# Performance work log

Measured on AMD Instinct MI355X. Metric: run time of the kernel, lower is better.

## Reference

```python
import jax, jax.numpy as jnp
import numpy as np
from jax import lax

T, B, C, H, W, NH = 4, 4, 512, 32, 32, 8
HD = C // NH  # head dim 64
EPS = 1e-5
TAU = 2.0

@jax.custom_vjp
def spike(x):
    # Heaviside forward (spikingjelly: x >= 0 -> 1)
    return (x >= 0.0).astype(x.dtype)

def _spike_fwd(x):
    return spike(x), x

def _spike_bwd(x, g):
    # sigmoid surrogate gradient, alpha=4.0 (spikingjelly default)
    s = jax.nn.sigmoid(4.0 * x)
    return (g * 4.0 * s * (1.0 - s),)

spike.defvjp(_spike_fwd, _spike_bwd)

def lif(x, v_th=1.0):
    # MultiStepLIFNode: tau=2, v_reset=0 (hard reset), detach_reset=True.
    # x: [T, ...]; sequential over T via scan.
    def step(v, xt):
        v = v + (xt - v) / TAU
        s = spike(v - v_th)
        v = v * (1.0 - lax.stop_gradient(s))  # detach_reset hard reset
        return v, s
    return lax.scan(step, jnp.zeros_like(x[0]), x)[1]

def bn(x, g, b, m, v):
    # eval-mode BatchNorm1d over channel axis 2 of [T,B,C,N]
    scale = g / jnp.sqrt(v + EPS)
    return (x - m[:, None]) * scale[:, None] + b[:, None]

def setup_inputs() -> dict:
    key = jax.random.key(0)
    ks = jax.random.split(key, 24)
    def w(k):
        return jax.random.normal(k, (C, C), jnp.float32) * (1.0 / np.sqrt(C))
    def bnp(k):
        k1, k2, k3, k4 = jax.random.split(k, 4)
        return (jax.random.normal(k1, (C,), jnp.float32) * 0.1 + 1.0,
                jax.random.normal(k2, (C,), jnp.float32) * 0.1,
                jax.random.normal(k3, (C,), jnp.float32) * 0.1,
                jax.random.uniform(k4, (C,), jnp.float32, 0.5, 1.5))
    q_g, q_b, q_m, q_v = bnp(ks[1])
    k_g, k_b, k_m, k_v = bnp(ks[3])
    v_g, v_b, v_m, v_v = bnp(ks[5])
    p_g, p_b, p_m, p_v = bnp(ks[7])
    return {
        'x': jax.random.normal(ks[0], (T, B, C, H, W), jnp.float32),
        'Wq': w(ks[10]), 'q_g': q_g, 'q_b': q_b, 'q_m': q_m, 'q_v': q_v,
        'Wk': w(ks[11]), 'k_g': k_g, 'k_b': k_b, 'k_m': k_m, 'k_v': k_v,
        'Wv': w(ks[12]), 'v_g': v_g, 'v_b': v_b, 'v_m': v_m, 'v_v': v_v,
        'Wp': w(ks[13]), 'bp': jax.random.normal(ks[14], (C,), jnp.float32) * 0.02,
        'p_g': p_g, 'p_b': p_b, 'p_m': p_m, 'p_v': p_v,
    }

def reference(x, Wq, q_g, q_b, q_m, q_v, Wk, k_g, k_b, k_m, k_v,
              Wv, v_g, v_b, v_m, v_v, Wp, bp, p_g, p_b, p_m, p_v):
    t, b, c, h, w = x.shape
    n = h * w
    xs = lif(x).reshape(t, b, c, n)  # proj_lif -> spikes in {0,1}

    def qkv_branch(Wt, g, bb, m, v):
        y = jnp.einsum('tbcn,dc->tbdn', xs, Wt)  # conv1x1
        y = lif(bn(y, g, bb, m, v))               # bn + lif
        # [T,B,C,N] -> [T,B,heads,N,head_dim]
        return y.reshape(t, b, NH, HD, n).transpose(0, 1, 2, 4, 3)

    q = qkv_branch(Wq, q_g, q_b, q_m, q_v)
    k = qkv_branch(Wk, k_g, k_b, k_m, k_v)
    v = qkv_branch(Wv, v_g, v_b, v_m, v_v)

    attn = jnp.einsum('tbhnd,tbhmd->tbhnm', q, k)           # q @ k^T (binary spikes)
    o = jnp.einsum('tbhnm,tbhmd->tbhnd', attn, v) * 0.125   # attn @ v * 0.125
    o = o.transpose(0, 1, 2, 4, 3).reshape(t, b, c, n)      # [T,B,C,N]
    o = lif(o, v_th=0.5)                                     # attn_lif

    y = jnp.einsum('tbcn,dc->tbdn', o, Wp) + bp[:, None]     # proj conv (bias)
    y = bn(y, p_g, p_b, p_m, p_v)
    return y.reshape(t, b, c, h, w)
```

## Files before the change

kernel.cpp:

```cpp
#include <hip/hip_runtime.h>
#include <hip/hip_bf16.h>
#include <stdint.h>

#define T_  4
#define B_  4
#define C_  512
#define N_  1024
#define NH_ 8
#define HD_ 64
#define NP_ 16384
#define EPS_ 1e-5f

typedef __bf16 bf16_t;
typedef __bf16 bf16x8 __attribute__((ext_vector_type(8)));
typedef float  f32x4  __attribute__((ext_vector_type(4)));
typedef unsigned short u16x4 __attribute__((ext_vector_type(4)));
typedef unsigned char  u8x4  __attribute__((ext_vector_type(4)));
typedef unsigned long long u64;
typedef unsigned int u32;

#define XS_OFF   0ULL
#define AHI_OFF  16777216ULL
#define ALO_OFF  18350080ULL
#define PHI_OFF  19922944ULL
#define PLO_OFF  20447232ULL
#define SC_OFF   20971520ULL
#define SH_OFF   20977664ULL
#define PSC_OFF  20983808ULL
#define PSH_OFF  20985856ULL
#define QS_OFF   20987904ULL
#define KB_OFF   37765120ULL
#define VB_OFF   38813696ULL
#define M2H_OFF  39862272ULL
#define M2L_OFF  40910848ULL

__global__ __launch_bounds__(256) void prep_kernel(
    const float* __restrict__ Wq, const float* __restrict__ Wk,
    const float* __restrict__ Wv, const float* __restrict__ Wp,
    const float* __restrict__ qg, const float* __restrict__ qb, const float* __restrict__ qm, const float* __restrict__ qv,
    const float* __restrict__ kg, const float* __restrict__ kb, const float* __restrict__ km, const float* __restrict__ kv,
    const float* __restrict__ vg, const float* __restrict__ vb, const float* __restrict__ vm, const float* __restrict__ vv,
    const float* __restrict__ bp,
    const float* __restrict__ pg, const float* __restrict__ pb, const float* __restrict__ pm, const float* __restrict__ pv,
    bf16_t* __restrict__ Ahi, bf16_t* __restrict__ Alo,
    bf16_t* __restrict__ Phi, bf16_t* __restrict__ Plo,
    float* __restrict__ scale, float* __restrict__ shift,
    float* __restrict__ pscale, float* __restrict__ pshift)
{
    const int i0 = blockIdx.x * 256 + threadIdx.x;
    const int stride = gridDim.x * 256;
    for (int idx = i0; idx < 1536 * 512; idx += stride) {
        int r = idx >> 9;
        int br = r >> 9;
        const float* W = (br == 0) ? Wq : (br == 1) ? Wk : Wv;
        float w = W[((r & 511) << 9) + (idx & 511)];
        bf16_t h = (bf16_t)w;
        Ahi[idx] = h;
        Alo[idx] = (bf16_t)(w - (float)h);
    }
    for (int idx = i0; idx < 512 * 512; idx += stride) {
        float w = Wp[idx];
        bf16_t h = (bf16_t)w;
        Phi[idx] = h;
        Plo[idx] = (bf16_t)(w - (float)h);
    }
    for (int idx = i0; idx < 1536; idx += stride) {
        int br = idx >> 9, d = idx & 511;
        const float* g  = (br == 0) ? qg : (br == 1) ? kg : vg;
        const float* bb = (br == 0) ? qb : (br == 1) ? kb : vb;
        const float* mm = (br == 0) ? qm : (br == 1) ? km : vm;
        const float* vr = (br == 0) ? qv : (br == 1) ? kv : vv;
        float sc = g[d] / sqrtf(vr[d] + EPS_);
        scale[idx] = sc;
        shift[idx] = bb[d] - mm[d] * sc;
    }
    for (int idx = i0; idx < 512; idx += stride) {
        float sc = pg[idx] / sqrtf(pv[idx] + EPS_);
        pscale[idx] = sc;
        pshift[idx] = (bp[idx] - pm[idx]) * sc + pb[idx];
    }
}

__global__ __launch_bounds__(256) void lif_x_kernel(const float* __restrict__ x,
                                                    bf16_t* __restrict__ xsT)
{
    __shared__ bf16_t St[64 * 72];
    const int tid = threadIdx.x;
    const int nl  = tid & 63;
    const int c4  = tid >> 6;
    const int n0 = blockIdx.x * 64;
    const int c0 = blockIdx.y * 64;
    const int b  = blockIdx.z;
    float v[16];
#pragma unroll
    for (int k = 0; k < 16; ++k) v[k] = 0.f;

    for (int t = 0; t < T_; ++t) {
        bf16x8 s0, s1;
#pragma unroll
        for (int k = 0; k < 16; ++k) {
            float xv = x[(size_t)((t * B_ + b) * C_ + (c0 + c4 * 16 + k)) * N_ + n0 + nl];
            float vn = v[k] + (xv - v[k]) * 0.5f;
            bool s = (vn >= 1.0f);
            v[k] = s ? 0.0f : vn;
            bf16_t sp = s ? (bf16_t)1.0f : (bf16_t)0.0f;
            if (k < 8) s0[k] = sp; else s1[k - 8] = sp;
        }
        __syncthreads();
        *(bf16x8*)&St[nl * 72 + c4 * 16]     = s0;
        *(bf16x8*)&St[nl * 72 + c4 * 16 + 8] = s1;
        __syncthreads();
#pragma unroll
        for (int it = 0; it < 2; ++it) {
            int id = it * 256 + tid;
            int row = id >> 3, sg = id & 7;
            *(bf16x8*)&xsT[((size_t)((t * B_ + b) << 10) + n0 + row) * C_ + c0 + sg * 8] =
                *(const bf16x8*)&St[row * 72 + sg * 8];
        }
    }
}

__global__ __launch_bounds__(256) void gemm_qkv_lif(
    const bf16_t* __restrict__ Ahi, const bf16_t* __restrict__ Alo,
    const bf16_t* __restrict__ xsT,
    const float* __restrict__ scale, const float* __restrict__ shift,
    bf16_t* __restrict__ qsT, u32* __restrict__ kbits, u32* __restrict__ vbits)
{
    __shared__ __align__(16) unsigned char smem[49152];

    const int tid  = threadIdx.x;
    const int lane = tid & 63;
    const int wv   = tid >> 6;
    const int wr   = wv >> 1, wc = wv & 1;
    const int m0   = blockIdx.y * 128;
    const int branch = m0 >> 9;
    const int site0 = blockIdx.x * 32;
    const int b    = site0 >> 10;
    const int n0   = site0 & 1023;

    const int frow = lane & 15;
    const int g4   = lane >> 4;

    f32x4 acc[4][4];
#pragma unroll
    for (int t = 0; t < 4; ++t)
#pragma unroll
        for (int mi = 0; mi < 4; ++mi) acc[t][mi] = f32x4{0.f, 0.f, 0.f, 0.f};

    for (int kk = 0; kk < 512; kk += 64) {
        __syncthreads();
#pragma unroll
        for (int p = 0; p < 4; ++p) {
            int s = p * 256 + tid;
            int row = s >> 3, j = s & 7;
            int kc = (j ^ (row & 7)) << 3;
            size_t goff = (size_t)(m0 + row) * 512 + kk + kc;
            unsigned ldsb = (unsigned)(p * 256 + wv * 64) * 16;
            __builtin_amdgcn_global_load_lds((const __attribute__((address_space(1))) void*)(Ahi + goff),
                                             (__attribute__((address_space(3))) void*)(smem + ldsb), 16, 0, 0);
            __builtin_amdgcn_global_load_lds((const __attribute__((address_space(1))) void*)(Alo + goff),
                                             (__attribute__((address_space(3))) void*)(smem + 16384 + ldsb), 16, 0, 0);
        }
#pragma unroll
        for (int p = 0; p < 4; ++p) {
            int s = p * 256 + tid;
            int t = s >> 8, row = (s >> 3) & 31, j = s & 7;
            int kc = (j ^ (row & 7)) << 3;
            size_t goff = ((size_t)((t * B_ + b) << 10) + n0 + row) * 512 + kk + kc;
            unsigned ldsb = 32768u + (unsigned)(p * 256 + wv * 64) * 16;
            __builtin_amdgcn_global_load_lds((const __attribute__((address_space(1))) void*)(xsT + goff),
                                             (__attribute__((address_space(3))) void*)(smem + ldsb), 16, 0, 0);
        }
        __syncthreads();

#pragma unroll
        for (int ks = 0; ks < 2; ++ks) {
            bf16x8 ah[4], al[4];
#pragma unroll
            for (int mi = 0; mi < 4; ++mi) {
                int row = wr * 64 + mi * 16 + frow;
                int jj = (ks * 4 + g4) ^ (row & 7);
                ah[mi] = *(const bf16x8*)(smem + row * 128 + jj * 16);
                al[mi] = *(const bf16x8*)(smem + 16384 + row * 128 + jj * 16);
            }
#pragma unroll
            for (int t = 0; t < 4; ++t) {
                int rowb = wc * 16 + frow;
                int jj = (ks * 4 + g4) ^ (rowb & 7);
                bf16x8 bb = *(const bf16x8*)(smem + 32768 + t * 4096 + rowb * 128 + jj * 16);
#pragma unroll
                for (int mi = 0; mi < 4; ++mi) {
                    acc[t][mi] = __builtin_amdgcn_mfma_f32_16x16x32_bf16(ah[mi], bb, acc[t][mi], 0, 0, 0);
                    acc[t][mi] = __builtin_amdgcn_mfma_f32_16x16x32_bf16(al[mi], bb, acc[t][mi], 0, 0, 0);
                }
            }
        }
    }

    if (branch == 0) {
        bf16_t* Tt = (bf16_t*)smem;
        u16x4 qpk[4][4];
#pragma unroll
        for (int mi = 0; mi < 4; ++mi)
#pragma unroll
            for (int r = 0; r < 4; ++r) {
                int gr = m0 + wr * 64 + mi * 16 + g4 * 4 + r;
                float sc = scale[gr], sh = shift[gr];
                float vv = 0.f;
#pragma unroll
                for (int t = 0; t < 4; ++t) {
                    float y = acc[t][mi][r] * sc + sh;
                    float vn = vv + (y - vv) * 0.5f;
                    bool s = (vn >= 1.0f);
                    vv = s ? 0.f : vn;
                    qpk[t][mi][r] = s ? 0x3F80 : 0;
                }
            }
#pragma unroll
        for (int t = 0; t < 4; ++t) {
            const int tb = t * B_ + b;
            __syncthreads();
#pragma unroll
            for (int mi = 0; mi < 4; ++mi) {
                int nl = wc * 16 + frow;
                int cl = wr * 64 + mi * 16 + g4 * 4;
                *(u16x4*)&Tt[nl * 136 + cl] = qpk[t][mi];
            }
            __syncthreads();
#pragma unroll
            for (int it = 0; it < 2; ++it) {
                int id = it * 256 + tid;
                int row = id >> 4, sg = id & 15;
                *(bf16x8*)&qsT[((size_t)(tb << 10) + n0 + row) * 512 + m0 + sg * 8] =
                    *(const bf16x8*)&Tt[row * 136 + sg * 8];
            }
        }
    } else {
        unsigned char* Sb = (unsigned char*)smem;
        u32* bdst = (branch == 1) ? kbits : vbits;
        u8x4 kpk[4][4];
#pragma unroll
        for (int mi = 0; mi < 4; ++mi)
#pragma unroll
            for (int r = 0; r < 4; ++r) {
                int gr = m0 + wr * 64 + mi * 16 + g4 * 4 + r;
                float sc = scale[gr], sh = shift[gr];
                float vv = 0.f;
#pragma unroll
                for (int t = 0; t < 4; ++t) {
                    float y = acc[t][mi][r] * sc + sh;
                    float vn = vv + (y - vv) * 0.5f;
                    bool s = (vn >= 1.0f);
                    vv = s ? 0.f : vn;
                    kpk[t][mi][r] = s ? 1 : 0;
                }
            }
#pragma unroll
        for (int t = 0; t < 4; ++t) {
            const int tb = t * B_ + b;
            __syncthreads();
#pragma unroll
            for (int mi = 0; mi < 4; ++mi) {
                int nl = wc * 16 + frow;
                int cl = wr * 64 + mi * 16 + g4 * 4;
                *(u8x4*)&Sb[nl * 132 + cl] = kpk[t][mi];
            }
            __syncthreads();
#pragma unroll
            for (int i = 0; i < 16; ++i) {
                int item = wv * 16 + i;
                int c = item * 2 + (lane >> 5);
                unsigned char vb_ = Sb[(lane & 31) * 132 + c];
                u64 mask = __ballot(vb_ != 0);
                if (lane == 0) {
                    int r0 = (m0 & 511) + item * 2;
                    int r1 = r0 + 1;
                    bdst[((size_t)(tb * NH_ + (r0 >> 6)) * 64 + (r0 & 63)) * 32 + (n0 >> 5)] = (u32)mask;
                    bdst[((size_t)(tb * NH_ + (r1 >> 6)) * 64 + (r1 & 63)) * 32 + (n0 >> 5)] = (u32)(mask >> 32);
                }
            }
        }
    }
}

__global__ __launch_bounds__(256) void gemm_proj(
    const bf16_t* __restrict__ Ahi, const bf16_t* __restrict__ Alo,
    const bf16_t* __restrict__ Bm,
    const float* __restrict__ scale, const float* __restrict__ shift,
    float* __restrict__ out)
{
    __shared__ bf16_t AsH[128 * 32];
    __shared__ bf16_t AsL[128 * 32];
    __shared__ bf16_t Bs [128 * 32];

    const int tid  = threadIdx.x;
    const int lane = tid & 63;
    const int wv   = tid >> 6;
    const int wr   = wv >> 1, wc = wv & 1;
    const int m0   = blockIdx.y * 128;
    const int n0   = blockIdx.x * 128;

    f32x4 acc[4][4];
#pragma unroll
    for (int i = 0; i < 4; ++i)
#pragma unroll
        for (int j = 0; j < 4; ++j) acc[i][j] = f32x4{0.f, 0.f, 0.f, 0.f};

    const int frow = lane & 15;
    const int koff = (lane >> 4) << 3;

    for (int kk = 0; kk < 512; kk += 32) {
#pragma unroll
        for (int s = 0; s < 2; ++s) {
            int idx = s * 256 + tid;
            int row = idx >> 2;
            int kc  = (idx & 3) << 3;
            size_t goffA = (size_t)(m0 + row) * 512 + kk + kc;
            size_t goffB = (size_t)(n0 + row) * 512 + kk + kc;
            int ldsoff = (s * 256 + wv * 64) * 8;
            __builtin_amdgcn_global_load_lds((const __attribute__((address_space(1))) void*)(Ahi + goffA),
                                             (__attribute__((address_space(3))) void*)(AsH + ldsoff), 16, 0, 0);
            __builtin_amdgcn_global_load_lds((const __attribute__((address_space(1))) void*)(Alo + goffA),
                                             (__attribute__((address_space(3))) void*)(AsL + ldsoff), 16, 0, 0);
            __builtin_amdgcn_global_load_lds((const __attribute__((address_space(1))) void*)(Bm + goffB),
                                             (__attribute__((address_space(3))) void*)(Bs + ldsoff), 16, 0, 0);
        }
        __syncthreads();

        bf16x8 ah[4], al[4], bb[4];
#pragma unroll
        for (int mi = 0; mi < 4; ++mi) {
            ah[mi] = *(const bf16x8*)&AsH[(wr * 64 + mi * 16 + frow) * 32 + koff];
            al[mi] = *(const bf16x8*)&AsL[(wr * 64 + mi * 16 + frow) * 32 + koff];
        }
#pragma unroll
        for (int ni = 0; ni < 4; ++ni)
            bb[ni] = *(const bf16x8*)&Bs[(wc * 64 + ni * 16 + frow) * 32 + koff];

#pragma unroll
        for (int mi = 0; mi < 4; ++mi)
#pragma unroll
            for (int ni = 0; ni < 4; ++ni) {
                acc[mi][ni] = __builtin_amdgcn_mfma_f32_16x16x32_bf16(ah[mi], bb[ni], acc[mi][ni], 0, 0, 0);
                acc[mi][ni] = __builtin_amdgcn_mfma_f32_16x16x32_bf16(al[mi], bb[ni], acc[mi][ni], 0, 0, 0);
            }
        __syncthreads();
    }

#pragma unroll
    for (int mi = 0; mi < 4; ++mi)
#pragma unroll
        for (int ni = 0; ni < 4; ++ni)
#pragma unroll
            for (int r = 0; r < 4; ++r) {
                int gr = m0 + wr * 64 + mi * 16 + (lane >> 4) * 4 + r;
                int gc = n0 + wc * 64 + ni * 16 + (lane & 15);
                float vout = acc[mi][ni][r] * scale[gr] + shift[gr];
                int tb = gc >> 10, nn = gc & 1023;
                out[((size_t)(tb * C_ + gr)) * N_ + nn] = vout;
            }
}

__global__ __launch_bounds__(256) void m2t_kernel(const u64* __restrict__ kbit,
                                                  const u64* __restrict__ vbit,
                                                  bf16_t* __restrict__ m2h,
                                                  bf16_t* __restrict__ m2l)
{
    __shared__ u64 Kb[64][17];
    __shared__ u64 Vb[64][17];
    __shared__ float M2f[64][64];
    const int tid = threadIdx.x;
    const int h  = blockIdx.x;
    const int tb = blockIdx.y;

    const u64* kbase = kbit + (size_t)(tb * NH_ + h) * 1024;
    const u64* vbase = vbit + (size_t)(tb * NH_ + h) * 1024;
    for (int i = tid; i < 1024; i += 256) {
        Kb[i >> 4][i & 15] = kbase[i];
        Vb[i >> 4][i & 15] = vbase[i];
    }
    __syncthreads();

    const int d1 = tid >> 2, l2 = tid & 3;
    int cnt[16];
#pragma unroll
    for (int jj = 0; jj < 16; ++jj) cnt[jj] = 0;
    for (int w = 0; w < 16; ++w) {
        u64 kw = Kb[d1][w];
#pragma unroll
        for (int jj = 0; jj < 16; ++jj)
            cnt[jj] += __popcll(kw & Vb[l2 + 4 * jj][w]);
    }
#pragma unroll
    for (int jj = 0; jj < 16; ++jj)
        M2f[d1][l2 + 4 * jj] = (float)cnt[jj] * 0.125f;
    __syncthreads();

    const int d2 = tid >> 2, d1b = (tid & 3) * 16;
    bf16x8 h0, h1, l0, l1;
#pragma unroll
    for (int j = 0; j < 16; ++j) {
        float m = M2f[d1b + j][d2];
        bf16_t hi = (bf16_t)m;
        bf16_t lo = (bf16_t)(m - (float)hi);
        if (j < 8) { h0[j] = hi; l0[j] = lo; } else { h1[j - 8] = hi; l1[j - 8] = lo; }
    }
    size_t base = (size_t)(tb * NH_ + h) * 4096 + tid * 16;
    *(bf16x8*)&m2h[base]     = h0;
    *(bf16x8*)&m2h[base + 8] = h1;
    *(bf16x8*)&m2l[base]     = l0;
    *(bf16x8*)&m2l[base + 8] = l1;
}

__global__ __launch_bounds__(256) void o_kernel(const bf16_t* __restrict__ qsT,
                                                const bf16_t* __restrict__ m2h,
                                                const bf16_t* __restrict__ m2l,
                                                bf16_t* __restrict__ osT)
{
    __shared__ bf16_t Ah[64][72];
    __shared__ bf16_t Al[64][72];
    __shared__ bf16_t Bq[128][72];

    const int tid  = threadIdx.x;
    const int lane = tid & 63;
    const int wv   = tid >> 6;
    const int nt = blockIdx.x, h = blockIdx.y, b = blockIdx.z;
    const int n0 = nt * 128;
    const int frow = lane & 15;
    const int g    = lane >> 4;

    float vst[4][2][4];
#pragma unroll
    for (int mi = 0; mi < 4; ++mi)
#pragma unroll
        for (int ni = 0; ni < 2; ++ni)
#pragma unroll
            for (int r = 0; r < 4; ++r) vst[mi][ni][r] = 0.f;

    for (int t = 0; t < T_; ++t) {
        const int tb = t * B_ + b;
        __syncthreads();
        {
            int row = tid >> 2, col = (tid & 3) * 16;
            size_t gbase = (size_t)(tb * NH_ + h) * 4096 + row * 64 + col;
            *(bf16x8*)&Ah[row][col]     = *(const bf16x8*)&m2h[gbase];
            *(bf16x8*)&Ah[row][col + 8] = *(const bf16x8*)&m2h[gbase + 8];
            *(bf16x8*)&Al[row][col]     = *(const bf16x8*)&m2l[gbase];
            *(bf16x8*)&Al[row][col + 8] = *(const bf16x8*)&m2l[gbase + 8];
        }
#pragma unroll
        for (int w = 0; w < 4; ++w) {
            int id = w * 256 + tid;
            int row = id >> 3, cg = (id & 7) * 8;
            *(bf16x8*)&Bq[row][cg] =
                *(const bf16x8*)&qsT[(size_t)((tb << 10) + n0 + row) * C_ + h * 64 + cg];
        }
        __syncthreads();

        bf16x8 afh[4][2], afl[4][2], bfq[2][2];
#pragma unroll
        for (int mi = 0; mi < 4; ++mi)
#pragma unroll
            for (int ks = 0; ks < 2; ++ks) {
                afh[mi][ks] = *(const bf16x8*)&Ah[mi * 16 + frow][ks * 32 + g * 8];
                afl[mi][ks] = *(const bf16x8*)&Al[mi * 16 + frow][ks * 32 + g * 8];
            }
#pragma unroll
        for (int ni = 0; ni < 2; ++ni)
#pragma unroll
            for (int ks = 0; ks < 2; ++ks)
                bfq[ni][ks] = *(const bf16x8*)&Bq[wv * 32 + ni * 16 + frow][ks * 32 + g * 8];

        f32x4 acc[4][2];
#pragma unroll
        for (int mi = 0; mi < 4; ++mi)
#pragma unroll
            for (int ni = 0; ni < 2; ++ni) acc[mi][ni] = f32x4{0.f, 0.f, 0.f, 0.f};

#pragma unroll
        for (int ks = 0; ks < 2; ++ks)
#pragma unroll
            for (int mi = 0; mi < 4; ++mi)
#pragma unroll
                for (int ni = 0; ni < 2; ++ni) {
                    acc[mi][ni] = __builtin_amdgcn_mfma_f32_16x16x32_bf16(afh[mi][ks], bfq[ni][ks], acc[mi][ni], 0, 0, 0);
                    acc[mi][ni] = __builtin_amdgcn_mfma_f32_16x16x32_bf16(afl[mi][ks], bfq[ni][ks], acc[mi][ni], 0, 0, 0);
                }

#pragma unroll
        for (int mi = 0; mi < 4; ++mi)
#pragma unroll
            for (int ni = 0; ni < 2; ++ni) {
                ushort4 pk;
                unsigned short* pp = &pk.x;
#pragma unroll
                for (int r = 0; r < 4; ++r) {
                    float o = acc[mi][ni][r];
                    float vn = vst[mi][ni][r] + (o - vst[mi][ni][r]) * 0.5f;
                    bool s = (vn >= 0.5f);
                    vst[mi][ni][r] = s ? 0.f : vn;
                    pp[r] = s ? 0x3F80 : 0;
                }
                size_t off = (size_t)((tb << 10) + n0 + wv * 32 + ni * 16 + frow) * C_
                           + h * 64 + mi * 16 + g * 4;
                *(ushort4*)&osT[off] = pk;
            }
    }
}

extern "C" void kernel_launch(void* const* d_in, const int* in_sizes, int n_in,
                              void* d_out, int out_size, void* d_ws, size_t ws_size,
                              hipStream_t stream)
{
    const float* x   = (const float*)d_in[0];
    const float* Wq  = (const float*)d_in[1];
    const float* qg  = (const float*)d_in[2];
    const float* qb  = (const float*)d_in[3];
    const float* qm  = (const float*)d_in[4];
    const float* qv  = (const float*)d_in[5];
    const float* Wk  = (const float*)d_in[6];
    const float* kg  = (const float*)d_in[7];
    const float* kb  = (const float*)d_in[8];
    const float* km  = (const float*)d_in[9];
    const float* kv  = (const float*)d_in[10];
    const float* Wv  = (const float*)d_in[11];
    const float* vg  = (const float*)d_in[12];
    const float* vb  = (const float*)d_in[13];
    const float* vm  = (const float*)d_in[14];
    const float* vv  = (const float*)d_in[15];
    const float* Wp  = (const float*)d_in[16];
    const float* bp  = (const float*)d_in[17];
    const float* pg  = (const float*)d_in[18];
    const float* pb  = (const float*)d_in[19];
    const float* pm  = (const float*)d_in[20];
    const float* pv  = (const float*)d_in[21];

    char* ws = (char*)d_ws;
    bf16_t* xsT    = (bf16_t*)(ws + XS_OFF);
    bf16_t* Ahi    = (bf16_t*)(ws + AHI_OFF);
    bf16_t* Alo    = (bf16_t*)(ws + ALO_OFF);
    bf16_t* Phi    = (bf16_t*)(ws + PHI_OFF);
    bf16_t* Plo    = (bf16_t*)(ws + PLO_OFF);
    float*  scv    = (float*)(ws + SC_OFF);
    float*  shv    = (float*)(ws + SH_OFF);
    float*  psc    = (float*)(ws + PSC_OFF);
    float*  psh    = (float*)(ws + PSH_OFF);
    bf16_t* qsT    = (bf16_t*)(ws + QS_OFF);
    u32*    kbits32= (u32*)(ws + KB_OFF);
    u32*    vbits32= (u32*)(ws + VB_OFF);
    u64*    kbits  = (u64*)(ws + KB_OFF);
    u64*    vbits  = (u64*)(ws + VB_OFF);
    bf16_t* m2h    = (bf16_t*)(ws + M2H_OFF);
    bf16_t* m2l    = (bf16_t*)(ws + M2L_OFF);
    bf16_t* osT    = (bf16_t*)(ws + XS_OFF);
    float*  out    = (float*)d_out;

    prep_kernel<<<dim3(3072), dim3(256), 0, stream>>>(
        Wq, Wk, Wv, Wp, qg, qb, qm, qv, kg, kb, km, kv, vg, vb, vm, vv,
        bp, pg, pb, pm, pv, Ahi, Alo, Phi, Plo, scv, shv, psc, psh);

    lif_x_kernel<<<dim3(16, 8, 4), dim3(256), 0, stream>>>(x, xsT);

    gemm_qkv_lif<<<dim3(128, 12), dim3(256), 0, stream>>>(
        Ahi, Alo, xsT, scv, shv, qsT, kbits32, vbits32);

    m2t_kernel<<<dim3(8, 16), dim3(256), 0, stream>>>(kbits, vbits, m2h, m2l);

    o_kernel<<<dim3(8, 8, 4), dim3(256), 0, stream>>>(qsT, m2h, m2l, osT);

    gemm_proj<<<dim3(128, 4), dim3(256), 0, stream>>>(Phi, Plo, osT, psc, psh, out);

    (void)in_sizes; (void)n_in; (void)out_size; (void)ws_size;
}
```

Baseline: 220.9 us.

## Double-buffer LDS staging in QKV and projection GEMMs with swizzled layouts

Both the QKV GEMM and the projection GEMM now use two LDS buffers, so the global_load_lds for k-step i+1 is issued before the MFMAs of step i run. This hides global-to-LDS latency and removes one barrier per iteration. The LDS tiles are repacked with XOR swizzles: the hi and lo A halves are interleaved per row, and the four timesteps of B are packed into one 256-byte row. This is meant to avoid bank conflicts. The K step of the QKV kernel drops from 64 to 32, which doubles its iteration count, and the projection kernel's LDS footprint grows to 48KB, which may reduce occupancy.

```diff
diff --git a/kernel.cpp b/kernel.cpp
--- a/kernel.cpp
+++ b/kernel.cpp
@@ -147,54 +147,63 @@
 #pragma unroll
         for (int mi = 0; mi < 4; ++mi) acc[t][mi] = f32x4{0.f, 0.f, 0.f, 0.f};
 
-    for (int kk = 0; kk < 512; kk += 64) {
-        __syncthreads();
+    auto stage = [&](int buf, int kk) {
+        unsigned char* Ab = smem + buf * 24576;
+        unsigned char* Bb = Ab + 16384;
 #pragma unroll
         for (int p = 0; p < 4; ++p) {
             int s = p * 256 + tid;
             int row = s >> 3, j = s & 7;
-            int kc = (j ^ (row & 7)) << 3;
-            size_t goff = (size_t)(m0 + row) * 512 + kk + kc;
-            unsigned ldsb = (unsigned)(p * 256 + wv * 64) * 16;
-            __builtin_amdgcn_global_load_lds((const __attribute__((address_space(1))) void*)(Ahi + goff),
-                                             (__attribute__((address_space(3))) void*)(smem + ldsb), 16, 0, 0);
-            __builtin_amdgcn_global_load_lds((const __attribute__((address_space(1))) void*)(Alo + goff),
-                                             (__attribute__((address_space(3))) void*)(smem + 16384 + ldsb), 16, 0, 0);
-        }
-#pragma unroll
-        for (int p = 0; p < 4; ++p) {
+            int jp = j ^ (row & 7);
+            const bf16_t* srcp = (jp & 4) ? Alo : Ahi;
+            size_t goff = (size_t)(m0 + row) * 512 + kk + (jp & 3) * 8;
+            __builtin_amdgcn_global_load_lds(
+                (const __attribute__((address_space(1))) void*)(srcp + goff),
+                (__attribute__((address_space(3))) void*)(Ab + (p * 256 + wv * 64) * 16), 16, 0, 0);
+        }
+#pragma unroll
+        for (int p = 0; p < 2; ++p) {
             int s = p * 256 + tid;
-            int t = s >> 8, row = (s >> 3) & 31, j = s & 7;
-            int kc = (j ^ (row & 7)) << 3;
-            size_t goff = ((size_t)((t * B_ + b) << 10) + n0 + row) * 512 + kk + kc;
-            unsigned ldsb = 32768u + (unsigned)(p * 256 + wv * 64) * 16;
-            __builtin_amdgcn_global_load_lds((const __attribute__((address_space(1))) void*)(xsT + goff),
-                                             (__attribute__((address_space(3))) void*)(smem + ldsb), 16, 0, 0);
+            int row = s >> 4, j = s & 15;
+            int jp = j ^ (row & 15);
+            int tt = jp & 3, c = jp >> 2;
+            size_t goff = ((size_t)((tt * B_ + b) << 10) + n0 + row) * 512 + kk + c * 8;
+            __builtin_amdgcn_global_load_lds(
+                (const __attribute__((address_space(1))) void*)(xsT + goff),
+                (__attribute__((address_space(3))) void*)(Bb + (p * 256 + wv * 64) * 16), 16, 0, 0);
+        }
+    };
+
+    stage(0, 0);
+    __syncthreads();
+    int cur = 0;
+    for (int step = 0; step < 16; ++step) {
+        if (step < 15) stage(cur ^ 1, (step + 1) * 32);
+
+        unsigned char* Ab = smem + cur * 24576;
+        unsigned char* Bb = Ab + 16384;
+        bf16x8 ah[4], al[4];
+#pragma unroll
+        for (int mi = 0; mi < 4; ++mi) {
+            int row = wr * 64 + mi * 16 + frow;
+            int jh = g4 ^ (row & 7);
+            int jl = (4 + g4) ^ (row & 7);
+            ah[mi] = *(const bf16x8*)(Ab + row * 128 + jh * 16);
+            al[mi] = *(const bf16x8*)(Ab + row * 128 + jl * 16);
+        }
+#pragma unroll
+        for (int t = 0; t < 4; ++t) {
+            int rowb = wc * 16 + frow;
+            int jb = (g4 * 4 + t) ^ (rowb & 15);
+            bf16x8 bb = *(const bf16x8*)(Bb + rowb * 256 + jb * 16);
+#pragma unroll
+            for (int mi = 0; mi < 4; ++mi) {
+                acc[t][mi] = __builtin_amdgcn_mfma_f32_16x16x32_bf16(ah[mi], bb, acc[t][mi], 0, 0, 0);
+                acc[t][mi] = __builtin_amdgcn_mfma_f32_16x16x32_bf16(al[mi], bb, acc[t][mi], 0, 0, 0);
+            }
         }
         __syncthreads();
-
-#pragma unroll
-        for (int ks = 0; ks < 2; ++ks) {
-            bf16x8 ah[4], al[4];
-#pragma unroll
-            for (int mi = 0; mi < 4; ++mi) {
-                int row = wr * 64 + mi * 16 + frow;
-                int jj = (ks * 4 + g4) ^ (row & 7);
-                ah[mi] = *(const bf16x8*)(smem + row * 128 + jj * 16);
-                al[mi] = *(const bf16x8*)(smem + 16384 + row * 128 + jj * 16);
-            }
-#pragma unroll
-            for (int t = 0; t < 4; ++t) {
-                int rowb = wc * 16 + frow;
-                int jj = (ks * 4 + g4) ^ (rowb & 7);
-                bf16x8 bb = *(const bf16x8*)(smem + 32768 + t * 4096 + rowb * 128 + jj * 16);
-#pragma unroll
-                for (int mi = 0; mi < 4; ++mi) {
-                    acc[t][mi] = __builtin_amdgcn_mfma_f32_16x16x32_bf16(ah[mi], bb, acc[t][mi], 0, 0, 0);
-                    acc[t][mi] = __builtin_amdgcn_mfma_f32_16x16x32_bf16(al[mi], bb, acc[t][mi], 0, 0, 0);
-                }
-            }
-        }
+        cur ^= 1;
     }
 
     if (branch == 0) {
@@ -284,14 +293,12 @@
 }
 
 __global__ __launch_bounds__(256) void gemm_proj(
-    const bf16_t* __restrict__ Ahi, const bf16_t* __restrict__ Alo,
+    const bf16_t* __restrict__ Phi, const bf16_t* __restrict__ Plo,
     const bf16_t* __restrict__ Bm,
     const float* __restrict__ scale, const float* __restrict__ shift,
     float* __restrict__ out)
 {
-    __shared__ bf16_t AsH[128 * 32];
-    __shared__ bf16_t AsL[128 * 32];
-    __shared__ bf16_t Bs [128 * 32];
+    __shared__ __align__(16) unsigned char smem[49152];
 
     const int tid  = threadIdx.x;
     const int lane = tid & 63;
@@ -300,43 +307,66 @@
     const int m0   = blockIdx.y * 128;
     const int n0   = blockIdx.x * 128;
 
+    const int frow = lane & 15;
+    const int g4   = lane >> 4;
+
     f32x4 acc[4][4];
 #pragma unroll
     for (int i = 0; i < 4; ++i)
 #pragma unroll
         for (int j = 0; j < 4; ++j) acc[i][j] = f32x4{0.f, 0.f, 0.f, 0.f};
 
-    const int frow = lane & 15;
-    const int koff = (lane >> 4) << 3;
-
-    for (int kk = 0; kk < 512; kk += 32) {
-#pragma unroll
-        for (int s = 0; s < 2; ++s) {
-            int idx = s * 256 + tid;
-            int row = idx >> 2;
-            int kc  = (idx & 3) << 3;
-            size_t goffA = (size_t)(m0 + row) * 512 + kk + kc;
-            size_t goffB = (size_t)(n0 + row) * 512 + kk + kc;
-            int ldsoff = (s * 256 + wv * 64) * 8;
-            __builtin_amdgcn_global_load_lds((const __attribute__((address_space(1))) void*)(Ahi + goffA),
-                                             (__attribute__((address_space(3))) void*)(AsH + ldsoff), 16, 0, 0);
-            __builtin_amdgcn_global_load_lds((const __attribute__((address_space(1))) void*)(Alo + goffA),
-                                             (__attribute__((address_space(3))) void*)(AsL + ldsoff), 16, 0, 0);
-            __builtin_amdgcn_global_load_lds((const __attribute__((address_space(1))) void*)(Bm + goffB),
-                                             (__attribute__((address_space(3))) void*)(Bs + ldsoff), 16, 0, 0);
-        }
-        __syncthreads();
-
+    auto stage = [&](int buf, int kk) {
+        unsigned char* Ab = smem + buf * 24576;
+        unsigned char* Bb = Ab + 16384;
+#pragma unroll
+        for (int p = 0; p < 4; ++p) {
+            int s = p * 256 + tid;
+            int row = s >> 3, j = s & 7;
+            int jp = j ^ (row & 7);
+            const bf16_t* srcp = (jp & 4) ? Plo : Phi;
+            size_t goff = (size_t)(m0 + row) * 512 + kk + (jp & 3) * 8;
+            __builtin_amdgcn_global_load_lds(
+                (const __attribute__((address_space(1))) void*)(srcp + goff),
+                (__attribute__((address_space(3))) void*)(Ab + (p * 256 + wv * 64) * 16), 16, 0, 0);
+        }
+#pragma unroll
+        for (int p = 0; p < 2; ++p) {
+            int s = p * 256 + tid;
+            int lr = s >> 3, j = s & 7;
+            int jp = j ^ (lr & 7);
+            int site = lr * 2 + (jp >> 2);
+            size_t goff = (size_t)(n0 + site) * 512 + kk + (jp & 3) * 8;
+            __builtin_amdgcn_global_load_lds(
+                (const __attribute__((address_space(1))) void*)(Bm + goff),
+                (__attribute__((address_space(3))) void*)(Bb + (p * 256 + wv * 64) * 16), 16, 0, 0);
+        }
+    };
+
+    stage(0, 0);
+    __syncthreads();
+    int cur = 0;
+    for (int step = 0; step < 16; ++step) {
+        if (step < 15) stage(cur ^ 1, (step + 1) * 32);
+
+        unsigned char* Ab = smem + cur * 24576;
+        unsigned char* Bb = Ab + 16384;
         bf16x8 ah[4], al[4], bb[4];
 #pragma unroll
         for (int mi = 0; mi < 4; ++mi) {
-            ah[mi] = *(const bf16x8*)&AsH[(wr * 64 + mi * 16 + frow) * 32 + koff];
-            al[mi] = *(const bf16x8*)&AsL[(wr * 64 + mi * 16 + frow) * 32 + koff];
-        }
-#pragma unroll
-        for (int ni = 0; ni < 4; ++ni)
-            bb[ni] = *(const bf16x8*)&Bs[(wc * 64 + ni * 16 + frow) * 32 + koff];
-
+            int row = wr * 64 + mi * 16 + frow;
+            int jh = g4 ^ (row & 7);
+            int jl = (4 + g4) ^ (row & 7);
+            ah[mi] = *(const bf16x8*)(Ab + row * 128 + jh * 16);
+            al[mi] = *(const bf16x8*)(Ab + row * 128 + jl * 16);
+        }
+#pragma unroll
+        for (int ni = 0; ni < 4; ++ni) {
+            int site = wc * 64 + ni * 16 + frow;
+            int lr = site >> 1;
+            int jb = ((site & 1) * 4 + g4) ^ (lr & 7);
+            bb[ni] = *(const bf16x8*)(Bb + lr * 128 + jb * 16);
+        }
 #pragma unroll
         for (int mi = 0; mi < 4; ++mi)
 #pragma unroll
@@ -345,6 +375,7 @@
                 acc[mi][ni] = __builtin_amdgcn_mfma_f32_16x16x32_bf16(al[mi], bb[ni], acc[mi][ni], 0, 0, 0);
             }
         __syncthreads();
+        cur ^= 1;
     }
 
 #pragma unroll
@@ -353,8 +384,8 @@
         for (int ni = 0; ni < 4; ++ni)
 #pragma unroll
             for (int r = 0; r < 4; ++r) {
-                int gr = m0 + wr * 64 + mi * 16 + (lane >> 4) * 4 + r;
-                int gc = n0 + wc * 64 + ni * 16 + (lane & 15);
+                int gr = m0 + wr * 64 + mi * 16 + g4 * 4 + r;
+                int gc = n0 + wc * 64 + ni * 16 + frow;
                 float vout = acc[mi][ni][r] * scale[gr] + shift[gr];
                 int tb = gc >> 10, nn = gc & 1023;
                 out[((size_t)(tb * C_ + gr)) * N_ + nn] = vout;
```

Measured after the change: 231.3 us. 4.7% more time.

## Widen gemm_proj K tile to 64 with XOR-swizzled LDS layout

Applied to the files above, without the earlier changes.

The projection GEMM now stages a 64-wide K slice per iteration instead of 32, halving the number of barrier-separated load/compute rounds. The hi, lo and B tiles now live in one 48KB shared buffer. Each 16-byte chunk is XOR-swizzled by row so the MFMA fragment reads from LDS avoid bank conflicts. The larger LDS footprint may lower occupancy, and there is still no double buffering.

```diff
diff --git a/kernel.cpp b/kernel.cpp
--- a/kernel.cpp
+++ b/kernel.cpp
@@ -284,14 +284,12 @@
 }
 
 __global__ __launch_bounds__(256) void gemm_proj(
-    const bf16_t* __restrict__ Ahi, const bf16_t* __restrict__ Alo,
+    const bf16_t* __restrict__ Phi, const bf16_t* __restrict__ Plo,
     const bf16_t* __restrict__ Bm,
     const float* __restrict__ scale, const float* __restrict__ shift,
     float* __restrict__ out)
 {
-    __shared__ bf16_t AsH[128 * 32];
-    __shared__ bf16_t AsL[128 * 32];
-    __shared__ bf16_t Bs [128 * 32];
+    __shared__ __align__(16) unsigned char smem[49152];
 
     const int tid  = threadIdx.x;
     const int lane = tid & 63;
@@ -300,61 +298,73 @@
     const int m0   = blockIdx.y * 128;
     const int n0   = blockIdx.x * 128;
 
+    const int frow = lane & 15;
+    const int g4   = lane >> 4;
+
     f32x4 acc[4][4];
 #pragma unroll
     for (int i = 0; i < 4; ++i)
 #pragma unroll
         for (int j = 0; j < 4; ++j) acc[i][j] = f32x4{0.f, 0.f, 0.f, 0.f};
 
-    const int frow = lane & 15;
-    const int koff = (lane >> 4) << 3;
-
-    for (int kk = 0; kk < 512; kk += 32) {
-#pragma unroll
-        for (int s = 0; s < 2; ++s) {
-            int idx = s * 256 + tid;
-            int row = idx >> 2;
-            int kc  = (idx & 3) << 3;
-            size_t goffA = (size_t)(m0 + row) * 512 + kk + kc;
-            size_t goffB = (size_t)(n0 + row) * 512 + kk + kc;
-            int ldsoff = (s * 256 + wv * 64) * 8;
-            __builtin_amdgcn_global_load_lds((const __attribute__((address_space(1))) void*)(Ahi + goffA),
-                                             (__attribute__((address_space(3))) void*)(AsH + ldsoff), 16, 0, 0);
-            __builtin_amdgcn_global_load_lds((const __attribute__((address_space(1))) void*)(Alo + goffA),
-                                             (__attribute__((address_space(3))) void*)(AsL + ldsoff), 16, 0, 0);
-            __builtin_amdgcn_global_load_lds((const __attribute__((address_space(1))) void*)(Bm + goffB),
-                                             (__attribute__((address_space(3))) void*)(Bs + ldsoff), 16, 0, 0);
-        }
-        __syncthreads();
-
-        bf16x8 ah[4], al[4], bb[4];
-#pragma unroll
-        for (int mi = 0; mi < 4; ++mi) {
-            ah[mi] = *(const bf16x8*)&AsH[(wr * 64 + mi * 16 + frow) * 32 + koff];
-            al[mi] = *(const bf16x8*)&AsL[(wr * 64 + mi * 16 + frow) * 32 + koff];
-        }
+    for (int kk = 0; kk < 512; kk += 64) {
+        __syncthreads();
+#pragma unroll
+        for (int p = 0; p < 4; ++p) {
+            int s = p * 256 + tid;
+            int row = s >> 3, j = s & 7;
+            int kc = (j ^ (row & 7)) << 3;
+            size_t goff = (size_t)(m0 + row) * 512 + kk + kc;
+            unsigned ldsb = (unsigned)(p * 256 + wv * 64) * 16;
+            __builtin_amdgcn_global_load_lds((const __attribute__((address_space(1))) void*)(Phi + goff),
+                                             (__attribute__((address_space(3))) void*)(smem + ldsb), 16, 0, 0);
+            __builtin_amdgcn_global_load_lds((const __attribute__((address_space(1))) void*)(Plo + goff),
+                                             (__attribute__((address_space(3))) void*)(smem + 16384 + ldsb), 16, 0, 0);
+        }
+#pragma unroll
+        for (int p = 0; p < 4; ++p) {
+            int s = p * 256 + tid;
+            int row = s >> 3, j = s & 7;
+            int kc = (j ^ (row & 7)) << 3;
+            size_t goff = (size_t)(n0 + row) * 512 + kk + kc;
+            unsigned ldsb = 32768u + (unsigned)(p * 256 + wv * 64) * 16;
+            __builtin_amdgcn_global_load_lds((const __attribute__((address_space(1))) void*)(Bm + goff),
+                                             (__attribute__((address_space(3))) void*)(smem + ldsb), 16, 0, 0);
+        }
+        __syncthreads();
+
+#pragma unroll
+        for (int ks = 0; ks < 2; ++ks) {
+            bf16x8 ah[4], al[4];
+#pragma unroll
+            for (int mi = 0; mi < 4; ++mi) {
+                int row = wr * 64 + mi * 16 + frow;
+                int jj = (ks * 4 + g4) ^ (row & 7);
+                ah[mi] = *(const bf16x8*)(smem + row * 128 + jj * 16);
+                al[mi] = *(const bf16x8*)(smem + 16384 + row * 128 + jj * 16);
+            }
+#pragma unroll
+            for (int ni = 0; ni < 4; ++ni) {
+                int site = wc * 64 + ni * 16 + frow;
+                int jj = (ks * 4 + g4) ^ (site & 7);
+                bf16x8 bb = *(const bf16x8*)(smem + 32768 + site * 128 + jj * 16);
+#pragma unroll
+                for (int mi = 0; mi < 4; ++mi) {
+                    acc[mi][ni] = __builtin_amdgcn_mfma_f32_16x16x32_bf16(ah[mi], bb, acc[mi][ni], 0, 0, 0);
+                    acc[mi][ni] = __builtin_amdgcn_mfma_f32_16x16x32_bf16(al[mi], bb, acc[mi][ni], 0, 0, 0);
+                }
+            }
+        }
+    }
+
+#pragma unroll
+    for (int mi = 0; mi < 4; ++mi)
 #pragma unroll
         for (int ni = 0; ni < 4; ++ni)
-            bb[ni] = *(const bf16x8*)&Bs[(wc * 64 + ni * 16 + frow) * 32 + koff];
-
-#pragma unroll
-        for (int mi = 0; mi < 4; ++mi)
-#pragma unroll
-            for (int ni = 0; ni < 4; ++ni) {
-                acc[mi][ni] = __builtin_amdgcn_mfma_f32_16x16x32_bf16(ah[mi], bb[ni], acc[mi][ni], 0, 0, 0);
-                acc[mi][ni] = __builtin_amdgcn_mfma_f32_16x16x32_bf16(al[mi], bb[ni], acc[mi][ni], 0, 0, 0);
-            }
-        __syncthreads();
-    }
-
-#pragma unroll
-    for (int mi = 0; mi < 4; ++mi)
-#pragma unroll
-        for (int ni = 0; ni < 4; ++ni)
 #pragma unroll
             for (int r = 0; r < 4; ++r) {
-                int gr = m0 + wr * 64 + mi * 16 + (lane >> 4) * 4 + r;
-                int gc = n0 + wc * 64 + ni * 16 + (lane & 15);
+                int gr = m0 + wr * 64 + mi * 16 + g4 * 4 + r;
+                int gc = n0 + wc * 64 + ni * 16 + frow;
                 float vout = acc[mi][ni][r] * scale[gr] + shift[gr];
                 int tb = gc >> 10, nn = gc & 1023;
                 out[((size_t)(tb * C_ + gr)) * N_ + nn] = vout;
```

New measurement: 216.6 us. Within noise of the previous version (-1.9%).
